# Optimization experiments

Measured on AMD Instinct MI355X. Metric: run time of the kernel, lower is better.

Reference implementation:

```python
import jax, jax.numpy as jnp
import numpy as np

B, T, D_MODEL, D_HIDDEN, MAX_SEQLEN = 4, 2048, 1024, 256, 2048


def setup_inputs() -> dict:
    key = jax.random.key(0)
    ks = jax.random.split(key, 8)
    s_in = 1.0 / np.sqrt(D_MODEL)
    s_out = 1.0 / np.sqrt(D_HIDDEN)
    # xavier_uniform bound for W_bias (fan_in = fan_out = MAX_SEQLEN)
    xb = np.sqrt(6.0 / (MAX_SEQLEN + MAX_SEQLEN))
    return {
        "q": jax.random.normal(ks[0], (B, T, D_MODEL), jnp.float32),
        "k": jax.random.normal(ks[1], (B, T, D_MODEL), jnp.float32),
        "v": jax.random.normal(ks[2], (B, T, D_MODEL), jnp.float32),
        "Wq": jax.random.normal(ks[3], (D_MODEL, D_HIDDEN), jnp.float32) * s_in,
        "Wk": jax.random.normal(ks[4], (D_MODEL, D_HIDDEN), jnp.float32) * s_in,
        "Wv": jax.random.normal(ks[5], (D_MODEL, D_HIDDEN), jnp.float32) * s_in,
        "Wo": jax.random.normal(ks[6], (D_HIDDEN, D_MODEL), jnp.float32) * s_out,
        "W_bias": jax.random.uniform(ks[7], (MAX_SEQLEN, MAX_SEQLEN), jnp.float32, -xb, xb),
    }


def reference(q, k, v, Wq, Wk, Wv, Wo, W_bias):
    Ti, Tj = q.shape[1], k.shape[1]
    Q = q @ Wq                      # [B,Ti,dh]
    K = k @ Wk                      # [B,Tj,dh]
    V = v @ Wv                      # [B,Tj,dh]
    pos_bias = W_bias[:Ti, :Tj][None]               # [1,Ti,Tj]
    # NOTE: source subtracts max over dim 0 (batch). For pos_bias that dim is 1,
    # so exp_pos_bias == exp(0) == ones -- reproduced faithfully here.
    max_key = jnp.max(K, axis=0, keepdims=True)      # [1,Tj,dh]
    max_pos_bias = jnp.max(pos_bias, axis=0, keepdims=True)
    exp_key = jnp.exp(K - max_key)                   # [B,Tj,dh]
    exp_pos_bias = jnp.exp(pos_bias - max_pos_bias)  # [1,Ti,Tj]
    num = jnp.einsum('ij,bjd->bid', exp_pos_bias[0], exp_key * V)  # [B,Ti,dh]
    den = jnp.einsum('ij,bjd->bid', exp_pos_bias[0], exp_key)      # [B,Ti,dh]
    Yt = jax.nn.sigmoid(Q) * num / den
    return Yt @ Wo                  # [B,Ti,d_model]
```

## Files before the change

### kernel.cpp

```cpp
#include <hip/hip_runtime.h>
#include <hip/hip_bf16.h>
#include <math.h>

#define B_   4
#define T_   2048
#define DM   1024
#define DH   256
#define M_   (B_*T_)

typedef __bf16 bf16;
typedef __attribute__((ext_vector_type(8))) __bf16 bf16x8;
typedef __attribute__((ext_vector_type(4))) float  f32x4;

#define LDT 72

__device__ inline float sigmoidf_(float x) { return 1.0f / (1.0f + __expf(-x)); }

__global__ void transpose_cvt_all(const float* __restrict__ Wq, const float* __restrict__ Wk,
                                  const float* __restrict__ Wv, const float* __restrict__ Wo,
                                  bf16* __restrict__ Wq_t, bf16* __restrict__ Wk_t,
                                  bf16* __restrict__ Wv_t, bf16* __restrict__ Wo_t,
                                  float* __restrict__ nd)
{
    const int bid = blockIdx.x;
    if (bid >= 1024) {
        nd[(bid - 1024) * 256 + threadIdx.x] = 0.f;
        return;
    }
    __shared__ float tile[32][33];
    const int w = bid >> 8, t = bid & 255;
    const float* in; bf16* out; int R, C, sh;
    if      (w == 0) { in = Wq; out = Wq_t; R = DM; C = DH; sh = 3; }
    else if (w == 1) { in = Wk; out = Wk_t; R = DM; C = DH; sh = 3; }
    else if (w == 2) { in = Wv; out = Wv_t; R = DM; C = DH; sh = 3; }
    else             { in = Wo; out = Wo_t; R = DH; C = DM; sh = 5; }
    const int r0 = (t >> sh) * 32, c0 = (t & ((1 << sh) - 1)) * 32;
    const int tx = threadIdx.x & 31, ty = threadIdx.x >> 5;
    #pragma unroll
    for (int i = ty; i < 32; i += 8)
        tile[i][tx] = in[(long)(r0 + i) * C + c0 + tx];
    __syncthreads();
    #pragma unroll
    for (int i = ty; i < 32; i += 8)
        out[(long)(c0 + i) * R + r0 + tx] = (bf16)tile[tx][i];
}

__global__ __launch_bounds__(512, 4)
void gemm_proj(const float* __restrict__ qin, const float* __restrict__ kin,
               const float* __restrict__ vin,
               const bf16* __restrict__ Wq_t, const bf16* __restrict__ Wk_t,
               const bf16* __restrict__ Wv_t,
               bf16* __restrict__ Yb, bf16* __restrict__ Kb, bf16* __restrict__ Vb)
{
    __shared__ __align__(16) bf16 As[64][LDT];
    __shared__ __align__(16) bf16 Bs[128][LDT];

    const int z = blockIdx.z;
    const float* A  = (z == 0) ? qin  : (z == 1) ? kin  : vin;
    const bf16*  Wt = (z == 0) ? Wq_t : (z == 1) ? Wk_t : Wv_t;
    bf16*        C  = (z == 0) ? Yb   : (z == 1) ? Kb   : Vb;

    const int m0 = blockIdx.x * 64;
    const int n0 = blockIdx.y * 128;
    const int tid = threadIdx.x, lane = tid & 63, wave = tid >> 6;
    const int wr = wave >> 2, wc = wave & 3;
    const int q4 = lane >> 4, l16 = lane & 15;

    f32x4 acc[2][2] = {};
    const int ar = tid >> 3, ac8 = (tid & 7) * 8;
    const int br = tid >> 2, bc16 = (tid & 3) * 16;

    const float* aBase = &A[(long)(m0 + ar) * DM + ac8];
    const bf16*  bBase = &Wt[(long)(n0 + br) * DM + bc16];

    f32x4  pa0[2], pa1[2];
    bf16x8 pb0[2], pb1[2];
    #pragma unroll
    for (int p = 0; p < 2; ++p) {
        const float* ap = aBase + p * 64;
        pa0[p] = *(const f32x4*)ap; pa1[p] = *(const f32x4*)(ap + 4);
        const bf16* bp = bBase + p * 64;
        pb0[p] = *(const bf16x8*)bp; pb1[p] = *(const bf16x8*)(bp + 8);
    }

    #pragma unroll
    for (int s = 0; s < 16; ++s) {
        const int p = s & 1;
        {   bf16x8 o;
            #pragma unroll
            for (int e = 0; e < 4; ++e) { o[e] = (bf16)pa0[p][e]; o[4 + e] = (bf16)pa1[p][e]; }
            *(bf16x8*)&As[ar][ac8]      = o;
            *(bf16x8*)&Bs[br][bc16]     = pb0[p];
            *(bf16x8*)&Bs[br][bc16 + 8] = pb1[p];
        }
        __syncthreads();
        if (s + 2 < 16) {
            const float* ap = aBase + (s + 2) * 64;
            pa0[p] = *(const f32x4*)ap; pa1[p] = *(const f32x4*)(ap + 4);
            const bf16* bp = bBase + (s + 2) * 64;
            pb0[p] = *(const bf16x8*)bp; pb1[p] = *(const bf16x8*)(bp + 8);
        }
        #pragma unroll
        for (int kk = 0; kk < 64; kk += 32) {
            bf16x8 a0 = *(const bf16x8*)&As[wr * 32      + l16][kk + q4 * 8];
            bf16x8 a1 = *(const bf16x8*)&As[wr * 32 + 16 + l16][kk + q4 * 8];
            bf16x8 b0 = *(const bf16x8*)&Bs[wc * 32      + l16][kk + q4 * 8];
            bf16x8 b1 = *(const bf16x8*)&Bs[wc * 32 + 16 + l16][kk + q4 * 8];
            acc[0][0] = __builtin_amdgcn_mfma_f32_16x16x32_bf16(a0, b0, acc[0][0], 0, 0, 0);
            acc[0][1] = __builtin_amdgcn_mfma_f32_16x16x32_bf16(a0, b1, acc[0][1], 0, 0, 0);
            acc[1][0] = __builtin_amdgcn_mfma_f32_16x16x32_bf16(a1, b0, acc[1][0], 0, 0, 0);
            acc[1][1] = __builtin_amdgcn_mfma_f32_16x16x32_bf16(a1, b1, acc[1][1], 0, 0, 0);
        }
        __syncthreads();
    }
    #pragma unroll
    for (int i = 0; i < 2; ++i)
        #pragma unroll
        for (int j = 0; j < 2; ++j)
            #pragma unroll
            for (int r = 0; r < 4; ++r) {
                int gm = m0 + wr * 32 + i * 16 + q4 * 4 + r;
                int gn = n0 + wc * 32 + j * 16 + l16;
                float v = acc[i][j][r];
                C[(long)gm * DH + gn] = (bf16)((z == 0) ? sigmoidf_(v) : v);
            }
}

__global__ void reduce_kv(const bf16* __restrict__ Kb, const bf16* __restrict__ Vb,
                          float* __restrict__ numb, float* __restrict__ denb)
{
    const int d  = threadIdx.x;
    const int j0 = blockIdx.x * 8;
    float sn[B_] = {0.f, 0.f, 0.f, 0.f};
    float sd[B_] = {0.f, 0.f, 0.f, 0.f};
    for (int jj = 0; jj < 8; ++jj) {
        int j = j0 + jj;
        float kv[B_], vv[B_], mx = -INFINITY;
        #pragma unroll
        for (int b = 0; b < B_; ++b) {
            kv[b] = (float)Kb[((long)b * T_ + j) * DH + d];
            vv[b] = (float)Vb[((long)b * T_ + j) * DH + d];
            mx = fmaxf(mx, kv[b]);
        }
        #pragma unroll
        for (int b = 0; b < B_; ++b) {
            float e = __expf(kv[b] - mx);
            sn[b] += e * vv[b];
            sd[b] += e;
        }
    }
    #pragma unroll
    for (int b = 0; b < B_; ++b) {
        atomicAdd(&numb[b * DH + d], sn[b]);
        atomicAdd(&denb[b * DH + d], sd[b]);
    }
}

__global__ __launch_bounds__(512, 4)
void gemm_out(const bf16* __restrict__ Yb, const bf16* __restrict__ Wo_t,
              const float* __restrict__ numb, const float* __restrict__ denb,
              float* __restrict__ out)
{
    __shared__ __align__(16) bf16 As[64][LDT];
    __shared__ __align__(16) bf16 Bs[128][LDT];
    __shared__ float rv_s[DH];

    const int m0 = blockIdx.x * 64;
    const int n0 = blockIdx.y * 128;
    const int b  = blockIdx.x >> 5;
    const int tid = threadIdx.x, lane = tid & 63, wave = tid >> 6;
    const int wr = wave >> 2, wc = wave & 3;
    const int q4 = lane >> 4, l16 = lane & 15;

    if (tid < DH) rv_s[tid] = numb[b * DH + tid] / denb[b * DH + tid];

    f32x4 acc[2][2] = {};
    const int ar = tid >> 3, ac8 = (tid & 7) * 8;
    const int br = tid >> 2, bc16 = (tid & 3) * 16;

    const bf16* aBase = &Yb[(long)(m0 + ar) * DH + ac8];
    const bf16* bBase = &Wo_t[(long)(n0 + br) * DH + bc16];

    bf16x8 pq[2], pb0[2], pb1[2];
    #pragma unroll
    for (int p = 0; p < 2; ++p) {
        pq[p]  = *(const bf16x8*)(aBase + p * 64);
        const bf16* wp = bBase + p * 64;
        pb0[p] = *(const bf16x8*)wp; pb1[p] = *(const bf16x8*)(wp + 8);
    }
    __syncthreads();

    #pragma unroll
    for (int s = 0; s < 4; ++s) {
        const int p = s & 1;
        {   bf16x8 o;
            #pragma unroll
            for (int e = 0; e < 8; ++e)
                o[e] = (bf16)((float)pq[p][e] * rv_s[s * 64 + ac8 + e]);
            *(bf16x8*)&As[ar][ac8]      = o;
            *(bf16x8*)&Bs[br][bc16]     = pb0[p];
            *(bf16x8*)&Bs[br][bc16 + 8] = pb1[p];
        }
        __syncthreads();
        if (s + 2 < 4) {
            pq[p]  = *(const bf16x8*)(aBase + (s + 2) * 64);
            const bf16* wp = bBase + (s + 2) * 64;
            pb0[p] = *(const bf16x8*)wp; pb1[p] = *(const bf16x8*)(wp + 8);
        }
        #pragma unroll
        for (int kk = 0; kk < 64; kk += 32) {
            bf16x8 a0 = *(const bf16x8*)&As[wr * 32      + l16][kk + q4 * 8];
            bf16x8 a1 = *(const bf16x8*)&As[wr * 32 + 16 + l16][kk + q4 * 8];
            bf16x8 b0 = *(const bf16x8*)&Bs[wc * 32      + l16][kk + q4 * 8];
            bf16x8 b1 = *(const bf16x8*)&Bs[wc * 32 + 16 + l16][kk + q4 * 8];
            acc[0][0] = __builtin_amdgcn_mfma_f32_16x16x32_bf16(a0, b0, acc[0][0], 0, 0, 0);
            acc[0][1] = __builtin_amdgcn_mfma_f32_16x16x32_bf16(a0, b1, acc[0][1], 0, 0, 0);
            acc[1][0] = __builtin_amdgcn_mfma_f32_16x16x32_bf16(a1, b0, acc[1][0], 0, 0, 0);
            acc[1][1] = __builtin_amdgcn_mfma_f32_16x16x32_bf16(a1, b1, acc[1][1], 0, 0, 0);
        }
        __syncthreads();
    }
    #pragma unroll
    for (int i = 0; i < 2; ++i)
        #pragma unroll
        for (int j = 0; j < 2; ++j)
            #pragma unroll
            for (int r = 0; r < 4; ++r) {
                int gm = m0 + wr * 32 + i * 16 + q4 * 4 + r;
                int gn = n0 + wc * 32 + j * 16 + l16;
                out[(long)gm * DM + gn] = acc[i][j][r];
            }
}

extern "C" void kernel_launch(void* const* d_in, const int* in_sizes, int n_in,
                              void* d_out, int out_size, void* d_ws, size_t ws_size,
                              hipStream_t stream)
{
    const float* q  = (const float*)d_in[0];
    const float* k  = (const float*)d_in[1];
    const float* v  = (const float*)d_in[2];
    const float* Wq = (const float*)d_in[3];
    const float* Wk = (const float*)d_in[4];
    const float* Wv = (const float*)d_in[5];
    const float* Wo = (const float*)d_in[6];
    float* out = (float*)d_out;

    char* ws = (char*)d_ws;
    bf16* Yb    = (bf16*)ws;  ws += (size_t)M_ * DH * sizeof(bf16);
    bf16* Kb    = (bf16*)ws;  ws += (size_t)M_ * DH * sizeof(bf16);
    bf16* Vb    = (bf16*)ws;  ws += (size_t)M_ * DH * sizeof(bf16);
    bf16* Wq_t  = (bf16*)ws;  ws += (size_t)DM * DH * sizeof(bf16);
    bf16* Wk_t  = (bf16*)ws;  ws += (size_t)DM * DH * sizeof(bf16);
    bf16* Wv_t  = (bf16*)ws;  ws += (size_t)DM * DH * sizeof(bf16);
    bf16* Wo_t  = (bf16*)ws;  ws += (size_t)DM * DH * sizeof(bf16);
    float* numb = (float*)ws; ws += (size_t)B_ * DH * sizeof(float);
    float* denb = (float*)ws; ws += (size_t)B_ * DH * sizeof(float);

    transpose_cvt_all<<<1032, 256, 0, stream>>>(Wq, Wk, Wv, Wo,
                                                Wq_t, Wk_t, Wv_t, Wo_t, numb);

    gemm_proj<<<dim3(M_ / 64, DH / 128, 3), 512, 0, stream>>>(q, k, v, Wq_t, Wk_t, Wv_t,
                                                              Yb, Kb, Vb);
    reduce_kv<<<256, 256, 0, stream>>>(Kb, Vb, numb, denb);
    gemm_out<<<dim3(M_ / 64, DM / 128), 512, 0, stream>>>(Yb, Wo_t, numb, denb, out);
}
```

Before: 197.2 us.

## Double-buffer swizzled LDS in GEMMs, remap tiles, vectorize KV reduction

Both GEMM kernels now use two LDS stages with an XOR swizzle instead of padded rows. The next stage is written while the current one is consumed, which drops one barrier per k-step. Block indices are remapped so neighbouring blocks spread across the tile grid, and the launch bounds hint moves from 4 to 6 blocks. reduce_kv now does 16-byte vector loads, combines partials with wave shuffles and shared memory, and issues fewer atomics. The costs are more LDS per block and more swizzle index arithmetic.

Measured after the change: 193.3 us. 1.02x faster.

```diff
diff --git a/kernel.cpp b/kernel.cpp
--- a/kernel.cpp
+++ b/kernel.cpp
@@ -12,9 +12,9 @@
 typedef __attribute__((ext_vector_type(8))) __bf16 bf16x8;
 typedef __attribute__((ext_vector_type(4))) float  f32x4;
 
-#define LDT 72
-
 __device__ inline float sigmoidf_(float x) { return 1.0f / (1.0f + __expf(-x)); }
+
+__device__ inline int swz8(int r, int c) { return (((c >> 3) ^ (r & 7)) << 3); }
 
 __global__ void transpose_cvt_all(const float* __restrict__ Wq, const float* __restrict__ Wk,
                                   const float* __restrict__ Wv, const float* __restrict__ Wo,
@@ -45,23 +45,26 @@
         out[(long)(c0 + i) * R + r0 + tx] = (bf16)tile[tx][i];
 }
 
-__global__ __launch_bounds__(512, 4)
+__global__ __launch_bounds__(512, 6)
 void gemm_proj(const float* __restrict__ qin, const float* __restrict__ kin,
                const float* __restrict__ vin,
                const bf16* __restrict__ Wq_t, const bf16* __restrict__ Wk_t,
                const bf16* __restrict__ Wv_t,
                bf16* __restrict__ Yb, bf16* __restrict__ Kb, bf16* __restrict__ Vb)
 {
-    __shared__ __align__(16) bf16 As[64][LDT];
-    __shared__ __align__(16) bf16 Bs[128][LDT];
+    __shared__ __align__(16) bf16 As[2][64][64];
+    __shared__ __align__(16) bf16 Bs[2][128][64];
 
     const int z = blockIdx.z;
     const float* A  = (z == 0) ? qin  : (z == 1) ? kin  : vin;
     const bf16*  Wt = (z == 0) ? Wq_t : (z == 1) ? Wk_t : Wv_t;
     bf16*        C  = (z == 0) ? Yb   : (z == 1) ? Kb   : Vb;
 
-    const int m0 = blockIdx.x * 64;
-    const int n0 = blockIdx.y * 128;
+    const int bid  = blockIdx.x;
+    const int tile = (bid & 7) * 32 + (bid >> 3);
+    const int m0 = (tile >> 1) * 64;
+    const int n0 = (tile & 1) * 128;
+
     const int tid = threadIdx.x, lane = tid & 63, wave = tid >> 6;
     const int wr = wave >> 2, wc = wave & 3;
     const int q4 = lane >> 4, l16 = lane & 15;
@@ -82,30 +85,41 @@
         const bf16* bp = bBase + p * 64;
         pb0[p] = *(const bf16x8*)bp; pb1[p] = *(const bf16x8*)(bp + 8);
     }
+    {
+        bf16x8 o;
+        #pragma unroll
+        for (int e = 0; e < 4; ++e) { o[e] = (bf16)pa0[0][e]; o[4 + e] = (bf16)pa1[0][e]; }
+        *(bf16x8*)&As[0][ar][swz8(ar, ac8)]      = o;
+        *(bf16x8*)&Bs[0][br][swz8(br, bc16)]     = pb0[0];
+        *(bf16x8*)&Bs[0][br][swz8(br, bc16 + 8)] = pb1[0];
+    }
+    __syncthreads();
 
     #pragma unroll
     for (int s = 0; s < 16; ++s) {
-        const int p = s & 1;
-        {   bf16x8 o;
-            #pragma unroll
-            for (int e = 0; e < 4; ++e) { o[e] = (bf16)pa0[p][e]; o[4 + e] = (bf16)pa1[p][e]; }
-            *(bf16x8*)&As[ar][ac8]      = o;
-            *(bf16x8*)&Bs[br][bc16]     = pb0[p];
-            *(bf16x8*)&Bs[br][bc16 + 8] = pb1[p];
-        }
-        __syncthreads();
+        const int cs = s & 1;
+        const int ns = cs ^ 1;
         if (s + 2 < 16) {
             const float* ap = aBase + (s + 2) * 64;
-            pa0[p] = *(const f32x4*)ap; pa1[p] = *(const f32x4*)(ap + 4);
+            pa0[cs] = *(const f32x4*)ap; pa1[cs] = *(const f32x4*)(ap + 4);
             const bf16* bp = bBase + (s + 2) * 64;
-            pb0[p] = *(const bf16x8*)bp; pb1[p] = *(const bf16x8*)(bp + 8);
+            pb0[cs] = *(const bf16x8*)bp; pb1[cs] = *(const bf16x8*)(bp + 8);
+        }
+        if (s + 1 < 16) {
+            bf16x8 o;
+            #pragma unroll
+            for (int e = 0; e < 4; ++e) { o[e] = (bf16)pa0[ns][e]; o[4 + e] = (bf16)pa1[ns][e]; }
+            *(bf16x8*)&As[ns][ar][swz8(ar, ac8)]      = o;
+            *(bf16x8*)&Bs[ns][br][swz8(br, bc16)]     = pb0[ns];
+            *(bf16x8*)&Bs[ns][br][swz8(br, bc16 + 8)] = pb1[ns];
         }
         #pragma unroll
         for (int kk = 0; kk < 64; kk += 32) {
-            bf16x8 a0 = *(const bf16x8*)&As[wr * 32      + l16][kk + q4 * 8];
-            bf16x8 a1 = *(const bf16x8*)&As[wr * 32 + 16 + l16][kk + q4 * 8];
-            bf16x8 b0 = *(const bf16x8*)&Bs[wc * 32      + l16][kk + q4 * 8];
-            bf16x8 b1 = *(const bf16x8*)&Bs[wc * 32 + 16 + l16][kk + q4 * 8];
+            const int ra = wr * 32 + l16, rb = wc * 32 + l16;
+            bf16x8 a0 = *(const bf16x8*)&As[cs][ra     ][swz8(ra,      kk + q4 * 8)];
+            bf16x8 a1 = *(const bf16x8*)&As[cs][ra + 16][swz8(ra + 16, kk + q4 * 8)];
+            bf16x8 b0 = *(const bf16x8*)&Bs[cs][rb     ][swz8(rb,      kk + q4 * 8)];
+            bf16x8 b1 = *(const bf16x8*)&Bs[cs][rb + 16][swz8(rb + 16, kk + q4 * 8)];
             acc[0][0] = __builtin_amdgcn_mfma_f32_16x16x32_bf16(a0, b0, acc[0][0], 0, 0, 0);
             acc[0][1] = __builtin_amdgcn_mfma_f32_16x16x32_bf16(a0, b1, acc[0][1], 0, 0, 0);
             acc[1][0] = __builtin_amdgcn_mfma_f32_16x16x32_bf16(a1, b0, acc[1][0], 0, 0, 0);
@@ -129,45 +143,74 @@
 __global__ void reduce_kv(const bf16* __restrict__ Kb, const bf16* __restrict__ Vb,
                           float* __restrict__ numb, float* __restrict__ denb)
 {
-    const int d  = threadIdx.x;
-    const int j0 = blockIdx.x * 8;
-    float sn[B_] = {0.f, 0.f, 0.f, 0.f};
-    float sd[B_] = {0.f, 0.f, 0.f, 0.f};
-    for (int jj = 0; jj < 8; ++jj) {
-        int j = j0 + jj;
-        float kv[B_], vv[B_], mx = -INFINITY;
-        #pragma unroll
-        for (int b = 0; b < B_; ++b) {
-            kv[b] = (float)Kb[((long)b * T_ + j) * DH + d];
-            vv[b] = (float)Vb[((long)b * T_ + j) * DH + d];
-            mx = fmaxf(mx, kv[b]);
-        }
-        #pragma unroll
-        for (int b = 0; b < B_; ++b) {
-            float e = __expf(kv[b] - mx);
-            sn[b] += e * vv[b];
-            sd[b] += e;
-        }
-    }
+    __shared__ float red[2][4][B_][DH];
+    const int tid = threadIdx.x;
+    const int g = tid & 31, jj = tid >> 5;
+    const int d8 = g * 8;
+    const int j = blockIdx.x * 8 + jj;
+
+    bf16x8 kx[B_], vx[B_];
     #pragma unroll
     for (int b = 0; b < B_; ++b) {
-        atomicAdd(&numb[b * DH + d], sn[b]);
-        atomicAdd(&denb[b * DH + d], sd[b]);
-    }
-}
-
-__global__ __launch_bounds__(512, 4)
+        kx[b] = *(const bf16x8*)&Kb[((long)b * T_ + j) * DH + d8];
+        vx[b] = *(const bf16x8*)&Vb[((long)b * T_ + j) * DH + d8];
+    }
+    float sn[B_][8], sd[B_][8];
+    #pragma unroll
+    for (int e = 0; e < 8; ++e) {
+        float k0 = (float)kx[0][e], k1 = (float)kx[1][e];
+        float k2 = (float)kx[2][e], k3 = (float)kx[3][e];
+        float mx = fmaxf(fmaxf(k0, k1), fmaxf(k2, k3));
+        float e0 = __expf(k0 - mx), e1 = __expf(k1 - mx);
+        float e2 = __expf(k2 - mx), e3 = __expf(k3 - mx);
+        sn[0][e] = e0 * (float)vx[0][e]; sd[0][e] = e0;
+        sn[1][e] = e1 * (float)vx[1][e]; sd[1][e] = e1;
+        sn[2][e] = e2 * (float)vx[2][e]; sd[2][e] = e2;
+        sn[3][e] = e3 * (float)vx[3][e]; sd[3][e] = e3;
+    }
+    #pragma unroll
+    for (int b = 0; b < B_; ++b)
+        #pragma unroll
+        for (int e = 0; e < 8; ++e) {
+            sn[b][e] += __shfl_xor(sn[b][e], 32);
+            sd[b][e] += __shfl_xor(sd[b][e], 32);
+        }
+    const int w = tid >> 6;
+    if ((tid & 32) == 0) {
+        #pragma unroll
+        for (int b = 0; b < B_; ++b)
+            #pragma unroll
+            for (int e = 0; e < 8; ++e) {
+                red[0][w][b][d8 + e] = sn[b][e];
+                red[1][w][b][d8 + e] = sd[b][e];
+            }
+    }
+    __syncthreads();
+    #pragma unroll
+    for (int o = tid; o < 2 * B_ * DH; o += 256) {
+        const int arr = o >> 10, b = (o >> 8) & 3, d = o & 255;
+        float s = red[arr][0][b][d] + red[arr][1][b][d]
+                + red[arr][2][b][d] + red[arr][3][b][d];
+        float* dst = (o < 1024) ? &numb[o] : &denb[o - 1024];
+        atomicAdd(dst, s);
+    }
+}
+
+__global__ __launch_bounds__(512, 6)
 void gemm_out(const bf16* __restrict__ Yb, const bf16* __restrict__ Wo_t,
               const float* __restrict__ numb, const float* __restrict__ denb,
               float* __restrict__ out)
 {
-    __shared__ __align__(16) bf16 As[64][LDT];
-    __shared__ __align__(16) bf16 Bs[128][LDT];
+    __shared__ __align__(16) bf16 As[2][64][64];
+    __shared__ __align__(16) bf16 Bs[2][128][64];
     __shared__ float rv_s[DH];
 
-    const int m0 = blockIdx.x * 64;
-    const int n0 = blockIdx.y * 128;
-    const int b  = blockIdx.x >> 5;
+    const int bid  = blockIdx.x;
+    const int tile = (bid & 7) * 128 + (bid >> 3);
+    const int m0 = (tile >> 3) * 64;
+    const int n0 = (tile & 7) * 128;
+    const int b  = m0 >> 11;
+
     const int tid = threadIdx.x, lane = tid & 63, wave = tid >> 6;
     const int wr = wave >> 2, wc = wave & 3;
     const int q4 = lane >> 4, l16 = lane & 15;
@@ -189,30 +232,41 @@
         pb0[p] = *(const bf16x8*)wp; pb1[p] = *(const bf16x8*)(wp + 8);
     }
     __syncthreads();
+    {
+        bf16x8 o;
+        #pragma unroll
+        for (int e = 0; e < 8; ++e)
+            o[e] = (bf16)((float)pq[0][e] * rv_s[ac8 + e]);
+        *(bf16x8*)&As[0][ar][swz8(ar, ac8)]      = o;
+        *(bf16x8*)&Bs[0][br][swz8(br, bc16)]     = pb0[0];
+        *(bf16x8*)&Bs[0][br][swz8(br, bc16 + 8)] = pb1[0];
+    }
+    __syncthreads();
 
     #pragma unroll
     for (int s = 0; s < 4; ++s) {
-        const int p = s & 1;
-        {   bf16x8 o;
+        const int cs = s & 1, ns = cs ^ 1;
+        if (s + 2 < 4) {
+            pq[cs]  = *(const bf16x8*)(aBase + (s + 2) * 64);
+            const bf16* wp = bBase + (s + 2) * 64;
+            pb0[cs] = *(const bf16x8*)wp; pb1[cs] = *(const bf16x8*)(wp + 8);
+        }
+        if (s + 1 < 4) {
+            bf16x8 o;
             #pragma unroll
             for (int e = 0; e < 8; ++e)
-                o[e] = (bf16)((float)pq[p][e] * rv_s[s * 64 + ac8 + e]);
-            *(bf16x8*)&As[ar][ac8]      = o;
-            *(bf16x8*)&Bs[br][bc16]     = pb0[p];
-            *(bf16x8*)&Bs[br][bc16 + 8] = pb1[p];
-        }
-        __syncthreads();
-        if (s + 2 < 4) {
-            pq[p]  = *(const bf16x8*)(aBase + (s + 2) * 64);
-            const bf16* wp = bBase + (s + 2) * 64;
-            pb0[p] = *(const bf16x8*)wp; pb1[p] = *(const bf16x8*)(wp + 8);
+                o[e] = (bf16)((float)pq[ns][e] * rv_s[(s + 1) * 64 + ac8 + e]);
+            *(bf16x8*)&As[ns][ar][swz8(ar, ac8)]      = o;
+            *(bf16x8*)&Bs[ns][br][swz8(br, bc16)]     = pb0[ns];
+            *(bf16x8*)&Bs[ns][br][swz8(br, bc16 + 8)] = pb1[ns];
         }
         #pragma unroll
         for (int kk = 0; kk < 64; kk += 32) {
-            bf16x8 a0 = *(const bf16x8*)&As[wr * 32      + l16][kk + q4 * 8];
-            bf16x8 a1 = *(const bf16x8*)&As[wr * 32 + 16 + l16][kk + q4 * 8];
-            bf16x8 b0 = *(const bf16x8*)&Bs[wc * 32      + l16][kk + q4 * 8];
-            bf16x8 b1 = *(const bf16x8*)&Bs[wc * 32 + 16 + l16][kk + q4 * 8];
+            const int ra = wr * 32 + l16, rb = wc * 32 + l16;
+            bf16x8 a0 = *(const bf16x8*)&As[cs][ra     ][swz8(ra,      kk + q4 * 8)];
+            bf16x8 a1 = *(const bf16x8*)&As[cs][ra + 16][swz8(ra + 16, kk + q4 * 8)];
+            bf16x8 b0 = *(const bf16x8*)&Bs[cs][rb     ][swz8(rb,      kk + q4 * 8)];
+            bf16x8 b1 = *(const bf16x8*)&Bs[cs][rb + 16][swz8(rb + 16, kk + q4 * 8)];
             acc[0][0] = __builtin_amdgcn_mfma_f32_16x16x32_bf16(a0, b0, acc[0][0], 0, 0, 0);
             acc[0][1] = __builtin_amdgcn_mfma_f32_16x16x32_bf16(a0, b1, acc[0][1], 0, 0, 0);
             acc[1][0] = __builtin_amdgcn_mfma_f32_16x16x32_bf16(a1, b0, acc[1][0], 0, 0, 0);
@@ -259,8 +313,8 @@
     transpose_cvt_all<<<1032, 256, 0, stream>>>(Wq, Wk, Wv, Wo,
                                                 Wq_t, Wk_t, Wv_t, Wo_t, numb);
 
-    gemm_proj<<<dim3(M_ / 64, DH / 128, 3), 512, 0, stream>>>(q, k, v, Wq_t, Wk_t, Wv_t,
-                                                              Yb, Kb, Vb);
+    gemm_proj<<<dim3(256, 1, 3), 512, 0, stream>>>(q, k, v, Wq_t, Wk_t, Wv_t,
+                                                   Yb, Kb, Vb);
     reduce_kv<<<256, 256, 0, stream>>>(Kb, Vb, numb, denb);
-    gemm_out<<<dim3(M_ / 64, DM / 128), 512, 0, stream>>>(Yb, Wo_t, numb, denb, out);
-}
+    gemm_out<<<1024, 512, 0, stream>>>(Yb, Wo_t, numb, denb, out);
+}
```
